# Kernel optimization log

Measured on AMD Instinct MI355X. Metric: run time of the kernel, lower is better.

The kernel has to match this reference:

```python
import jax, jax.numpy as jnp
import numpy as np

N = 50000      # nodes (patients)
E = 500000     # directed edges
H = 128        # Config.HIDDEN_DIM
GH = 256       # Config.GRAPH_HIDDEN
C = 14         # Config.NUM_CLASSES


def setup_inputs() -> dict:
    key = jax.random.key(0)
    ks = jax.random.split(key, 24)
    s = 0.02
    inp = {
        "h_v": jax.random.normal(ks[0], (N, H), jnp.float32),
        "h_t": jax.random.normal(ks[1], (N, H), jnp.float32),
        "h_tab": jax.random.normal(ks[2], (N, H), jnp.float32),
        "edge_index": jax.random.randint(ks[3], (2, E), 0, N, jnp.int64),
        # SAGEConv1: in=3H, out=GH  (lin_l on mean-aggr neighbors w/ bias, lin_r on root, no bias)
        "W1l": jax.random.normal(ks[4], (3 * H, GH), jnp.float32) * s,
        "W1r": jax.random.normal(ks[5], (3 * H, GH), jnp.float32) * s,
        "b1g": jnp.zeros((GH,), jnp.float32),
        # SAGEConv2: in=GH, out=H
        "W2l": jax.random.normal(ks[6], (GH, H), jnp.float32) * s,
        "W2r": jax.random.normal(ks[7], (GH, H), jnp.float32) * s,
        "b2g": jnp.zeros((H,), jnp.float32),
        # projections H->H
        "Wsh": jax.random.normal(ks[8], (H, H), jnp.float32) * s,
        "bsh": jnp.zeros((H,), jnp.float32),
        "Wst": jax.random.normal(ks[9], (H, H), jnp.float32) * s,
        "bst": jnp.zeros((H,), jnp.float32),
        "Wstab": jax.random.normal(ks[10], (H, H), jnp.float32) * s,
        "bstab": jnp.zeros((H,), jnp.float32),
        # classifier 4H -> 256 -> C
        "Wc1": jax.random.normal(ks[11], (4 * H, 256), jnp.float32) * s,
        "bc1": jnp.zeros((256,), jnp.float32),
        "Wc2": jax.random.normal(ks[12], (256, C), jnp.float32) * s,
        "bc2": jnp.zeros((C,), jnp.float32),
    }
    return inp


def _sage_conv(x, src, dst, Wl, Wr, b):
    # PyG SAGEConv with mean aggregation (eval mode):
    # out = mean_{j in N(i)} x_j @ Wl + b  +  x_i @ Wr
    n = x.shape[0]
    agg = jax.ops.segment_sum(x[src], dst, num_segments=n)          # [N, d_in]
    cnt = jax.ops.segment_sum(jnp.ones((src.shape[0],), x.dtype), dst, num_segments=n)
    mean = agg / jnp.maximum(cnt, 1.0)[:, None]
    return mean @ Wl + b + x @ Wr


def reference(h_v, h_t, h_tab, edge_index,
              W1l, W1r, b1g, W2l, W2r, b2g,
              Wsh, bsh, Wst, bst, Wstab, bstab,
              Wc1, bc1, Wc2, bc2):
    src, dst = edge_index[0], edge_index[1]
    node_feats = jnp.concatenate([h_v, h_t, h_tab], axis=1)          # [N, 3H]
    h_g = jax.nn.relu(_sage_conv(node_feats, src, dst, W1l, W1r, b1g))
    h_g = _sage_conv(h_g, src, dst, W2l, W2r, b2g)                   # [N, H]
    # F.normalize(p=2, dim=1)
    h_g = h_g / jnp.maximum(jnp.linalg.norm(h_g, axis=1, keepdims=True), 1e-12)
    z_shared = h_g @ Wsh + bsh
    z_t = h_t @ Wst + bst
    z_tab = h_tab @ Wstab + bstab
    combined = jnp.concatenate([z_shared, z_t, z_tab, h_g], axis=1)  # [N, 4H]
    logits = jax.nn.relu(combined @ Wc1 + bc1) @ Wc2 + bc2           # [N, C]
    return (logits, z_shared, z_t, z_tab)
```

## Files before the change

kernel.cpp:

```cpp
#include <hip/hip_runtime.h>
#include <math.h>

typedef __attribute__((ext_vector_type(8))) short short8;
typedef __attribute__((ext_vector_type(4))) float f32x4;
typedef __attribute__((ext_vector_type(4))) unsigned int u32x4;

static __device__ __forceinline__ unsigned short f2bf(float f) {
    union { float f; unsigned int u; } v; v.f = f;
    unsigned int r = v.u + 0x7fffu + ((v.u >> 16) & 1u);
    return (unsigned short)(r >> 16);
}
static __device__ __forceinline__ float bflo(unsigned int u) {
    union { unsigned int u; float f; } v; v.u = u << 16; return v.f;
}
static __device__ __forceinline__ float bfhi(unsigned int u) {
    union { unsigned int u; float f; } v; v.u = u & 0xffff0000u; return v.f;
}

typedef __attribute__((address_space(1))) const unsigned int gu32;
typedef __attribute__((address_space(3))) unsigned int lu32;
static __device__ __forceinline__ void gload16(const void* g, void* l) {
    __builtin_amdgcn_global_load_lds((gu32*)g, (lu32*)l, 16, 0, 0);
}

__global__ void convert_x(const float* __restrict__ hv, const float* __restrict__ ht,
                          const float* __restrict__ htab, unsigned short* __restrict__ X,
                          int total )
{
    int idx = blockIdx.x * blockDim.x + threadIdx.x;
    if (idx >= total) return;
    int r = idx / 96;
    int c4 = idx - r * 96;
    int seg = c4 >> 5;
    const float* s = (seg == 0) ? hv : (seg == 1) ? ht : htab;
    float4 v = ((const float4*)s)[(size_t)r * 32 + (c4 & 31)];
    ushort4 o;
    o.x = f2bf(v.x); o.y = f2bf(v.y); o.z = f2bf(v.z); o.w = f2bf(v.w);
    *(ushort4*)(X + (size_t)r * 384 + c4 * 4) = o;
}

struct WDesc { const float* src; int K; int N; int dstoff; };
struct WPack { WDesc w[9]; };
__global__ void convert_w(WPack p, unsigned short* __restrict__ dst)
{
    WDesc d = p.w[blockIdx.y];
    int total = d.K * d.N;
    for (int i = blockIdx.x * blockDim.x + threadIdx.x; i < total;
         i += gridDim.x * blockDim.x) {
        int k = i / d.N, n = i - k * d.N;
        dst[d.dstoff + (size_t)n * d.K + k] = f2bf(d.src[i]);
    }
}

struct GemmP {
    const unsigned short* A; int lda;
    const unsigned short* Bt;
    const float* bias;
    float* Cf; int ldcf;
    unsigned short* Cb; int ldcb;
};
struct GemmP3 { GemmP q[3]; };

template<int MODE, int NP>
__global__ __launch_bounds__(256, 4) void gemm4(GemmP3 ps, int M, int K)
{
    __shared__ __align__(16) unsigned short smem[128 * 64 * 2];
    unsigned short* As = smem;
    unsigned short* Bs = smem + 128 * 64;
    const GemmP P = ps.q[(MODE == 1) ? blockIdx.z : 0];
    const int tid = threadIdx.x;
    const int lane = tid & 63;
    const int wid = tid >> 6;
    const int wr = wid >> 1, wc = wid & 1;
    const int bid = blockIdx.x;
    const int q = bid >> 3;
    const int m0 = ((bid & 7) + 8 * (q / NP)) * 128;
    const int n0 = (q % NP) * 128;

    const int lrow = lane >> 3;
    const int lchk = (lane & 7) ^ lrow;
    const unsigned short* gA[4];
    #pragma unroll
    for (int i = 0; i < 4; ++i) {
        int r = m0 + wid * 32 + i * 8 + lrow;
        if (r > M - 1) r = M - 1;
        gA[i] = P.A + (size_t)r * P.lda + lchk * 8;
    }
    const unsigned short* gB[4];
    #pragma unroll
    for (int i = 0; i < 4; ++i) {
        int r = n0 + wid * 32 + i * 8 + lrow;
        gB[i] = P.Bt + (size_t)r * K + lchk * 8;
    }
    unsigned short* lA = As + wid * 32 * 64;
    unsigned short* lB = Bs + wid * 32 * 64;

    f32x4 acc[4][4] = {};
    const int nt = K >> 6;
    for (int t = 0; t < nt; ++t) {
        __syncthreads();
        #pragma unroll
        for (int i = 0; i < 4; ++i) gload16(gA[i] + t * 64, lA + i * 8 * 64);
        #pragma unroll
        for (int i = 0; i < 4; ++i) gload16(gB[i] + t * 64, lB + i * 8 * 64);
        asm volatile("s_waitcnt vmcnt(0)" ::: "memory");
        __syncthreads();
        #pragma unroll
        for (int kk = 0; kk < 2; ++kk) {
            int g = kk * 4 + (lane >> 4);
            short8 a[4], b[4];
            #pragma unroll
            for (int mi = 0; mi < 4; ++mi) {
                int row = wr * 64 + mi * 16 + (lane & 15);
                a[mi] = *(const short8*)(As + row * 64 + ((g ^ (row & 7)) * 8));
            }
            #pragma unroll
            for (int ni = 0; ni < 4; ++ni) {
                int row = wc * 64 + ni * 16 + (lane & 15);
                b[ni] = *(const short8*)(Bs + row * 64 + ((g ^ (row & 7)) * 8));
            }
            #pragma unroll
            for (int mi = 0; mi < 4; ++mi)
                #pragma unroll
                for (int ni = 0; ni < 4; ++ni)
                    acc[mi][ni] = __builtin_amdgcn_mfma_f32_16x16x32_bf16(
                        a[mi], b[ni], acc[mi][ni], 0, 0, 0);
        }
    }

    if (MODE == 0) {
        unsigned short* stage = smem;
        #pragma unroll
        for (int half = 0; half < 2; ++half) {
            __syncthreads();
            if (wr == half) {
                #pragma unroll
                for (int mi = 0; mi < 4; ++mi)
                    #pragma unroll
                    for (int ni = 0; ni < 4; ++ni) {
                        int colL = wc * 64 + ni * 16 + (lane & 15);
                        #pragma unroll
                        for (int j = 0; j < 4; ++j) {
                            int rel = mi * 16 + ((lane >> 4) << 2) + j;
                            stage[rel * 128 + colL] = f2bf(acc[mi][ni][j]);
                        }
                    }
            }
            __syncthreads();
            #pragma unroll
            for (int p = 0; p < 4; ++p) {
                int idx = p * 256 + tid;
                int r = idx >> 4, c8 = idx & 15;
                int grow = m0 + half * 64 + r;
                if (grow < M)
                    __builtin_nontemporal_store(
                        *(const u32x4*)(stage + r * 128 + c8 * 8),
                        (u32x4*)(P.Cb + (size_t)grow * P.ldcb + n0 + c8 * 8));
            }
        }
    }

    if (MODE == 1) {
        __syncthreads();
        #pragma unroll
        for (int mi = 0; mi < 4; ++mi)
            #pragma unroll
            for (int ni = 0; ni < 4; ++ni) {
                int colL = wc * 64 + ni * 16 + (lane & 15);
                float bv = P.bias[colL];
                #pragma unroll
                for (int j = 0; j < 4; ++j) {
                    int rL = wr * 64 + mi * 16 + ((lane >> 4) << 2) + j;
                    smem[rL * 128 + colL] = f2bf(acc[mi][ni][j] + bv);
                }
            }
        __syncthreads();
        #pragma unroll
        for (int p = 0; p < 8; ++p) {
            int idx = p * 256 + tid;
            int r = idx >> 4, c8 = idx & 15;
            int grow = m0 + r;
            if (grow < M)
                __builtin_nontemporal_store(
                    *(const u32x4*)(smem + r * 128 + c8 * 8),
                    (u32x4*)(P.Cb + (size_t)grow * P.ldcb + n0 + c8 * 8));
        }
        float* stagef = (float*)smem;
        #pragma unroll
        for (int half = 0; half < 2; ++half) {
            __syncthreads();
            if (wr == half) {
                #pragma unroll
                for (int mi = 0; mi < 4; ++mi)
                    #pragma unroll
                    for (int ni = 0; ni < 4; ++ni) {
                        int colL = wc * 64 + ni * 16 + (lane & 15);
                        float bv = P.bias[colL];
                        #pragma unroll
                        for (int j = 0; j < 4; ++j) {
                            int rel = mi * 16 + ((lane >> 4) << 2) + j;
                            stagef[rel * 128 + colL] = acc[mi][ni][j] + bv;
                        }
                    }
            }
            __syncthreads();
            #pragma unroll
            for (int p = 0; p < 8; ++p) {
                int idx = p * 256 + tid;
                int r = idx >> 5, c4 = idx & 31;
                int grow = m0 + half * 64 + r;
                if (grow < M)
                    __builtin_nontemporal_store(
                        *(const f32x4*)(stagef + r * 128 + c4 * 4),
                        (f32x4*)(P.Cf + (size_t)grow * P.ldcf + n0 + c4 * 4));
            }
        }
    }
}

__global__ __launch_bounds__(512, 2) void gemm5(
    const unsigned short* __restrict__ A,
    const unsigned short* __restrict__ Bt,
    const float* __restrict__ bias,
    const unsigned short* __restrict__ Wc2t,
    const float* __restrict__ bc2,
    float* __restrict__ logits,
    int M, int K)
{
    __shared__ __align__(16) unsigned short smem[128 * 256];
    unsigned short* As = smem;
    unsigned short* Bs = smem + 128 * 64;
    const int tid = threadIdx.x;
    const int lane = tid & 63;
    const int wid = tid >> 6;
    const int wr = wid >> 2;
    const int wc = wid & 3;
    const int m0 = blockIdx.x * 128;

    const int lrow = lane >> 3;
    const int lchk = (lane & 7) ^ lrow;
    const unsigned short* gA[2];
    #pragma unroll
    for (int i = 0; i < 2; ++i) {
        int r = m0 + wid * 16 + i * 8 + lrow;
        if (r > M - 1) r = M - 1;
        gA[i] = A + (size_t)r * K + lchk * 8;
    }
    const unsigned short* gB[4];
    #pragma unroll
    for (int i = 0; i < 4; ++i) {
        int r = wid * 32 + i * 8 + lrow;
        gB[i] = Bt + (size_t)r * K + lchk * 8;
    }
    unsigned short* lA = As + wid * 16 * 64;
    unsigned short* lB = Bs + wid * 32 * 64;

    f32x4 acc[4][4] = {};
    const int nt = K >> 6;
    for (int t = 0; t < nt; ++t) {
        __syncthreads();
        #pragma unroll
        for (int i = 0; i < 2; ++i) gload16(gA[i] + t * 64, lA + i * 8 * 64);
        #pragma unroll
        for (int i = 0; i < 4; ++i) gload16(gB[i] + t * 64, lB + i * 8 * 64);
        asm volatile("s_waitcnt vmcnt(0)" ::: "memory");
        __syncthreads();
        #pragma unroll
        for (int kk = 0; kk < 2; ++kk) {
            int g = kk * 4 + (lane >> 4);
            short8 a[4], b[4];
            #pragma unroll
            for (int mi = 0; mi < 4; ++mi) {
                int row = wr * 64 + mi * 16 + (lane & 15);
                a[mi] = *(const short8*)(As + row * 64 + ((g ^ (row & 7)) * 8));
            }
            #pragma unroll
            for (int ni = 0; ni < 4; ++ni) {
                int row = wc * 64 + ni * 16 + (lane & 15);
                b[ni] = *(const short8*)(Bs + row * 64 + ((g ^ (row & 7)) * 8));
            }
            #pragma unroll
            for (int mi = 0; mi < 4; ++mi)
                #pragma unroll
                for (int ni = 0; ni < 4; ++ni)
                    acc[mi][ni] = __builtin_amdgcn_mfma_f32_16x16x32_bf16(
                        a[mi], b[ni], acc[mi][ni], 0, 0, 0);
        }
    }

    __syncthreads();
    #pragma unroll
    for (int mi = 0; mi < 4; ++mi)
        #pragma unroll
        for (int ni = 0; ni < 4; ++ni) {
            int colL = wc * 64 + ni * 16 + (lane & 15);
            float bv = bias[colL];
            #pragma unroll
            for (int j = 0; j < 4; ++j) {
                int rL = wr * 64 + mi * 16 + ((lane >> 4) << 2) + j;
                float x = fmaxf(acc[mi][ni][j] + bv, 0.0f);
                int c8 = colL >> 3;
                smem[rL * 256 + ((c8 ^ (rL & 7)) * 8) + (colL & 7)] = f2bf(x);
            }
        }
    __syncthreads();
    f32x4 lacc = {0.f, 0.f, 0.f, 0.f};
    int rL = wid * 16 + (lane & 15);
    #pragma unroll
    for (int k0 = 0; k0 < 256; k0 += 32) {
        int c8 = (k0 >> 3) + (lane >> 4);
        short8 a = *(const short8*)(smem + rL * 256 + ((c8 ^ (rL & 7)) * 8));
        short8 b = *(const short8*)(Wc2t + (lane & 15) * 256 + k0 + (lane >> 4) * 8);
        lacc = __builtin_amdgcn_mfma_f32_16x16x32_bf16(a, b, lacc, 0, 0, 0);
    }
    int colL = lane & 15;
    if (colL < 14) {
        float bb = bc2[colL];
        #pragma unroll
        for (int j = 0; j < 4; ++j) {
            int r = m0 + wid * 16 + (lane >> 4) * 4 + j;
            if (r < M)
                __builtin_nontemporal_store(lacc[j] + bb,
                    logits + (size_t)r * 14 + colL);
        }
    }
}

__global__ void count_deg(const int* __restrict__ dst, int* __restrict__ deg, int E)
{
    int e = blockIdx.x * blockDim.x + threadIdx.x;
    if (e < E) atomicAdd(&deg[dst[e]], 1);
}

__global__ __launch_bounds__(1024) void scan_part(
    const int* __restrict__ deg, int* __restrict__ off, int* __restrict__ sums, int N)
{
    __shared__ int buf[1024];
    int i = blockIdx.x * 1024 + threadIdx.x;
    int v = (i < N) ? deg[i] : 0;
    buf[threadIdx.x] = v;
    __syncthreads();
    #pragma unroll
    for (int o = 1; o < 1024; o <<= 1) {
        int t = (threadIdx.x >= o) ? buf[threadIdx.x - o] : 0;
        __syncthreads();
        buf[threadIdx.x] += t;
        __syncthreads();
    }
    if (i < N) off[i] = buf[threadIdx.x] - v;
    if (threadIdx.x == 1023) sums[blockIdx.x] = buf[1023];
}

__global__ void scan_sums(int* __restrict__ sums, int* __restrict__ offN, int nb)
{
    int lane = threadIdx.x;
    int v = (lane < nb) ? sums[lane] : 0;
    int incl = v;
    #pragma unroll
    for (int o = 1; o < 64; o <<= 1) {
        int t = __shfl_up(incl, o);
        if (lane >= o) incl += t;
    }
    if (lane < nb) sums[lane] = incl - v;
    if (lane == 63) *offN = incl;
}

__global__ __launch_bounds__(1024) void scan_add(
    const int* __restrict__ sums, int* __restrict__ off,
    int* __restrict__ cursor, int N)
{
    int i = blockIdx.x * 1024 + threadIdx.x;
    if (i < N) {
        int v = off[i] + sums[blockIdx.x];
        off[i] = v;
        cursor[i] = v;
    }
}

__global__ void fill_csr(const int* __restrict__ src, const int* __restrict__ dst,
                         int* __restrict__ cursor, int* __restrict__ csr, int E)
{
    int e = blockIdx.x * blockDim.x + threadIdx.x;
    if (e < E) {
        int p = atomicAdd(&cursor[dst[e]], 1);
        csr[p] = src[e];
    }
}

__global__ __launch_bounds__(256) void sage1_gather(
    const unsigned short* __restrict__ y1,
    const int* __restrict__ off, const int* __restrict__ csr,
    const float* __restrict__ b, unsigned short* __restrict__ out, int N)
{
    int lane = threadIdx.x & 63;
    int node = blockIdx.x * 4 + (threadIdx.x >> 6);
    if (node >= N) return;
    int s = off[node], e = off[node + 1];
    int half = lane >> 5, l32 = lane & 31;
    float a[8] = {};
    int p = s + half;
    for (; p + 6 < e; p += 8) {
        int j0 = csr[p],     j1 = csr[p + 2];
        int j2 = csr[p + 4], j3 = csr[p + 6];
        uint4 v0 = *(const uint4*)(y1 + (size_t)j0 * 512 + l32 * 8);
        uint4 v1 = *(const uint4*)(y1 + (size_t)j1 * 512 + l32 * 8);
        uint4 v2 = *(const uint4*)(y1 + (size_t)j2 * 512 + l32 * 8);
        uint4 v3 = *(const uint4*)(y1 + (size_t)j3 * 512 + l32 * 8);
        a[0] += bflo(v0.x); a[1] += bfhi(v0.x); a[2] += bflo(v0.y); a[3] += bfhi(v0.y);
        a[4] += bflo(v0.z); a[5] += bfhi(v0.z); a[6] += bflo(v0.w); a[7] += bfhi(v0.w);
        a[0] += bflo(v1.x); a[1] += bfhi(v1.x); a[2] += bflo(v1.y); a[3] += bfhi(v1.y);
        a[4] += bflo(v1.z); a[5] += bfhi(v1.z); a[6] += bflo(v1.w); a[7] += bfhi(v1.w);
        a[0] += bflo(v2.x); a[1] += bfhi(v2.x); a[2] += bflo(v2.y); a[3] += bfhi(v2.y);
        a[4] += bflo(v2.z); a[5] += bfhi(v2.z); a[6] += bflo(v2.w); a[7] += bfhi(v2.w);
        a[0] += bflo(v3.x); a[1] += bfhi(v3.x); a[2] += bflo(v3.y); a[3] += bfhi(v3.y);
        a[4] += bflo(v3.z); a[5] += bfhi(v3.z); a[6] += bflo(v3.w); a[7] += bfhi(v3.w);
    }
    for (; p + 2 < e; p += 4) {
        int j0 = csr[p], j1 = csr[p + 2];
        uint4 v0 = *(const uint4*)(y1 + (size_t)j0 * 512 + l32 * 8);
        uint4 v1 = *(const uint4*)(y1 + (size_t)j1 * 512 + l32 * 8);
        a[0] += bflo(v0.x); a[1] += bfhi(v0.x); a[2] += bflo(v0.y); a[3] += bfhi(v0.y);
        a[4] += bflo(v0.z); a[5] += bfhi(v0.z); a[6] += bflo(v0.w); a[7] += bfhi(v0.w);
        a[0] += bflo(v1.x); a[1] += bfhi(v1.x); a[2] += bflo(v1.y); a[3] += bfhi(v1.y);
        a[4] += bflo(v1.z); a[5] += bfhi(v1.z); a[6] += bflo(v1.w); a[7] += bfhi(v1.w);
    }
    for (; p < e; p += 2) {
        int j = csr[p];
        uint4 v = *(const uint4*)(y1 + (size_t)j * 512 + l32 * 8);
        a[0] += bflo(v.x); a[1] += bfhi(v.x); a[2] += bflo(v.y); a[3] += bfhi(v.y);
        a[4] += bflo(v.z); a[5] += bfhi(v.z); a[6] += bflo(v.w); a[7] += bfhi(v.w);
    }
    #pragma unroll
    for (int i = 0; i < 8; ++i) a[i] += __shfl_xor(a[i], 32);
    if (half == 0) {
        float inv = (e > s) ? 1.0f / (float)(e - s) : 1.0f;
        uint4 rv = *(const uint4*)(y1 + (size_t)node * 512 + 256 + l32 * 8);
        float4 b0 = ((const float4*)b)[l32 * 2];
        float4 b1 = ((const float4*)b)[l32 * 2 + 1];
        float r[8] = {bflo(rv.x), bfhi(rv.x), bflo(rv.y), bfhi(rv.y),
                      bflo(rv.z), bfhi(rv.z), bflo(rv.w), bfhi(rv.w)};
        float bb[8] = {b0.x, b0.y, b0.z, b0.w, b1.x, b1.y, b1.z, b1.w};
        u32x4 vv;
        #pragma unroll
        for (int i = 0; i < 4; ++i) {
            unsigned int lo = f2bf(fmaxf(a[2*i]   * inv + bb[2*i]   + r[2*i],   0.f));
            unsigned int hi = f2bf(fmaxf(a[2*i+1] * inv + bb[2*i+1] + r[2*i+1], 0.f));
            vv[i] = lo | (hi << 16);
        }
        __builtin_nontemporal_store(vv, (u32x4*)(out + (size_t)node * 256 + l32 * 8));
    }
}

__global__ __launch_bounds__(256) void sage2_gather_norm(
    const unsigned short* __restrict__ y2,
    const int* __restrict__ off, const int* __restrict__ csr,
    const float* __restrict__ b, unsigned short* __restrict__ outb, int N)
{
    int lane = threadIdx.x & 63;
    int node = blockIdx.x * 4 + (threadIdx.x >> 6);
    if (node >= N) return;
    int s = off[node], e = off[node + 1];
    int grp = lane >> 4, l16 = lane & 15;
    float a[8] = {};
    int p = s + grp;
    for (; p + 4 < e; p += 8) {
        int j0 = csr[p], j1 = csr[p + 4];
        uint4 v0 = *(const uint4*)(y2 + (size_t)j0 * 256 + l16 * 8);
        uint4 v1 = *(const uint4*)(y2 + (size_t)j1 * 256 + l16 * 8);
        a[0] += bflo(v0.x); a[1] += bfhi(v0.x); a[2] += bflo(v0.y); a[3] += bfhi(v0.y);
        a[4] += bflo(v0.z); a[5] += bfhi(v0.z); a[6] += bflo(v0.w); a[7] += bfhi(v0.w);
        a[0] += bflo(v1.x); a[1] += bfhi(v1.x); a[2] += bflo(v1.y); a[3] += bfhi(v1.y);
        a[4] += bflo(v1.z); a[5] += bfhi(v1.z); a[6] += bflo(v1.w); a[7] += bfhi(v1.w);
    }
    for (; p < e; p += 4) {
        int j = csr[p];
        uint4 v = *(const uint4*)(y2 + (size_t)j * 256 + l16 * 8);
        a[0] += bflo(v.x); a[1] += bfhi(v.x); a[2] += bflo(v.y); a[3] += bfhi(v.y);
        a[4] += bflo(v.z); a[5] += bfhi(v.z); a[6] += bflo(v.w); a[7] += bfhi(v.w);
    }
    #pragma unroll
    for (int i = 0; i < 8; ++i) {
        a[i] += __shfl_xor(a[i], 16);
        a[i] += __shfl_xor(a[i], 32);
    }
    if (grp == 0) {
        float inv = (e > s) ? 1.0f / (float)(e - s) : 1.0f;
        uint4 rv = *(const uint4*)(y2 + (size_t)node * 256 + 128 + l16 * 8);
        float4 b0 = ((const float4*)b)[l16 * 2];
        float4 b1 = ((const float4*)b)[l16 * 2 + 1];
        float r[8] = {bflo(rv.x), bfhi(rv.x), bflo(rv.y), bfhi(rv.y),
                      bflo(rv.z), bfhi(rv.z), bflo(rv.w), bfhi(rv.w)};
        float bb[8] = {b0.x, b0.y, b0.z, b0.w, b1.x, b1.y, b1.z, b1.w};
        float h[8];
        float ss = 0.f;
        #pragma unroll
        for (int i = 0; i < 8; ++i) {
            h[i] = a[i] * inv + bb[i] + r[i];
            ss += h[i] * h[i];
        }
        ss += __shfl_xor(ss, 1);
        ss += __shfl_xor(ss, 2);
        ss += __shfl_xor(ss, 4);
        ss += __shfl_xor(ss, 8);
        float sc = 1.0f / fmaxf(sqrtf(ss), 1e-12f);
        u32x4 vv;
        #pragma unroll
        for (int i = 0; i < 4; ++i) {
            unsigned int lo = f2bf(h[2*i] * sc);
            unsigned int hi = f2bf(h[2*i+1] * sc);
            vv[i] = lo | (hi << 16);
        }
        __builtin_nontemporal_store(vv, (u32x4*)(outb + (size_t)node * 512 + l16 * 8));
    }
}

extern "C" void kernel_launch(void* const* d_in, const int* in_sizes, int n_in,
                              void* d_out, int out_size, void* d_ws, size_t ws_size,
                              hipStream_t stream)
{
    const float* h_v   = (const float*)d_in[0];
    const float* h_t   = (const float*)d_in[1];
    const float* h_tab = (const float*)d_in[2];
    const int*   eidx  = (const int*)d_in[3];
    const float* W1l = (const float*)d_in[4];
    const float* W1r = (const float*)d_in[5];
    const float* b1g = (const float*)d_in[6];
    const float* W2l = (const float*)d_in[7];
    const float* W2r = (const float*)d_in[8];
    const float* b2g = (const float*)d_in[9];
    const float* Wsh = (const float*)d_in[10];
    const float* bsh = (const float*)d_in[11];
    const float* Wst = (const float*)d_in[12];
    const float* bst = (const float*)d_in[13];
    const float* Wstab = (const float*)d_in[14];
    const float* bstab = (const float*)d_in[15];
    const float* Wc1 = (const float*)d_in[16];
    const float* bc1 = (const float*)d_in[17];
    const float* Wc2 = (const float*)d_in[18];
    const float* bc2 = (const float*)d_in[19];

    const int N = in_sizes[0] / 128;
    const int E = in_sizes[3] / 2;
    const int* src = eidx;
    const int* dst = eidx + E;

    int* deg    = (int*)d_ws;
    int* off    = deg + N;
    int* cursor = off + N + 1;
    int* csr    = cursor + N;
    int* sums   = csr + E;
    size_t int_bytes = ((size_t)3 * N + 1 + E + 64) * 4;
    unsigned short* Wt = (unsigned short*)((char*)d_ws + ((int_bytes + 255) & ~(size_t)255));
    const int oW1l = 0;
    const int oW1r = oW1l + 98304;
    const int oW2l = oW1r + 98304;
    const int oW2r = oW2l + 32768;
    const int oWsh = oW2r + 32768;
    const int oWst = oWsh + 16384;
    const int oWstab = oWst + 16384;
    const int oWc1 = oWstab + 16384;
    const int oWc2t = oWc1 + 131072;
    const int wtotal = oWc2t + 4096;

    unsigned short* Xbf   = Wt + wtotal;
    unsigned short* bufY  = Xbf + (size_t)N * 384;
    unsigned short* bufH  = bufY + (size_t)N * 512;
    unsigned short* bufY2 = bufH + (size_t)N * 256;

    float* out    = (float*)d_out;
    float* logits = out;
    float* z_sh   = out + (size_t)N * 14;
    float* z_t    = z_sh + (size_t)N * 128;
    float* z_tab  = z_t + (size_t)N * 128;

    const int gx = (N + 127) / 128;
    const int gxp = (gx + 7) & ~7;
    const int nb = (N + 1023) / 1024;

    hipMemsetAsync(deg, 0, (size_t)N * 4, stream);
    hipMemsetAsync(Wt + oWc2t, 0, 16 * 256 * 2, stream);
    count_deg<<<(E + 255) / 256, 256, 0, stream>>>(dst, deg, E);
    scan_part<<<nb, 1024, 0, stream>>>(deg, off, sums, N);
    scan_sums<<<1, 64, 0, stream>>>(sums, off + N, nb);
    scan_add<<<nb, 1024, 0, stream>>>(sums, off, cursor, N);
    fill_csr<<<(E + 255) / 256, 256, 0, stream>>>(src, dst, cursor, csr, E);

    convert_x<<<(N * 96 + 255) / 256, 256, 0, stream>>>(h_v, h_t, h_tab, Xbf, N * 96);
    WPack p;
    p.w[0] = {W1l, 384, 256, oW1l};     p.w[1] = {W1r, 384, 256, oW1r};
    p.w[2] = {W2l, 256, 128, oW2l};     p.w[3] = {W2r, 256, 128, oW2r};
    p.w[4] = {Wsh, 128, 128, oWsh};     p.w[5] = {Wst, 128, 128, oWst};
    p.w[6] = {Wstab, 128, 128, oWstab}; p.w[7] = {Wc1, 512, 256, oWc1};
    p.w[8] = {Wc2, 256, 14, oWc2t};
    convert_w<<<dim3(128, 9), 256, 0, stream>>>(p, Wt);

    unsigned short* y1 = bufY;
    {
        GemmP3 g{};
        g.q[0] = {Xbf, 384, Wt + oW1l, nullptr, nullptr, 0, y1, 512};
        gemm4<0, 4><<<dim3(gxp * 4), 256, 0, stream>>>(g, N, 384);
    }

    sage1_gather<<<(N + 3) / 4, 256, 0, stream>>>(y1, off, csr, b1g, bufH, N);

    {
        GemmP3 g{};
        g.q[0] = {bufH, 256, Wt + oW2l, nullptr, nullptr, 0, bufY2, 256};
        gemm4<0, 2><<<dim3(gxp * 2), 256, 0, stream>>>(g, N, 256);
    }

    unsigned short* cls_bf = bufY;
    sage2_gather_norm<<<(N + 3) / 4, 256, 0, stream>>>(bufY2, off, csr, b2g,
        cls_bf + 384, N);

    {
        GemmP3 g{};
        g.q[0] = {cls_bf + 384, 512, Wt + oWsh,   bsh,   z_sh,  128, cls_bf + 0,   512};
        g.q[1] = {Xbf + 128,    384, Wt + oWst,   bst,   z_t,   128, cls_bf + 128, 512};
        g.q[2] = {Xbf + 256,    384, Wt + oWstab, bstab, z_tab, 128, cls_bf + 256, 512};
        gemm4<1, 1><<<dim3(gxp, 1, 3), 256, 0, stream>>>(g, N, 128);
    }

    gemm5<<<dim3(gxp), 512, 0, stream>>>(cls_bf, Wt + oWc1, bc1,
        Wt + oWc2t, bc2, logits, N, 512);
}
```

Before: 265.9 us.

## Fuse projection GEMMs into classifier kernel, keeping z tiles in shared memory

Merges the three H->H projection GEMMs (z_shared, z_t, z_tab) into the classifier kernel. Each block computes a 128-row z tile, writes it to global in fp32, keeps a bf16 copy in LDS, and immediately accumulates it into the first classifier layer. This removes one launch and the bf16 round-trip of the combined feature buffer through global memory. In exchange, the projections now run serially inside one block per row tile, with more barriers and no overlap between loads and MFMA, which lowers parallelism in that stage.

```diff
diff --git a/kernel.cpp b/kernel.cpp
--- a/kernel.cpp
+++ b/kernel.cpp
@@ -67,7 +67,7 @@
     __shared__ __align__(16) unsigned short smem[128 * 64 * 2];
     unsigned short* As = smem;
     unsigned short* Bs = smem + 128 * 64;
-    const GemmP P = ps.q[(MODE == 1) ? blockIdx.z : 0];
+    const GemmP P = ps.q[0];
     const int tid = threadIdx.x;
     const int lane = tid & 63;
     const int wid = tid >> 6;
@@ -128,141 +128,215 @@
         }
     }
 
-    if (MODE == 0) {
-        unsigned short* stage = smem;
-        #pragma unroll
-        for (int half = 0; half < 2; ++half) {
-            __syncthreads();
-            if (wr == half) {
-                #pragma unroll
-                for (int mi = 0; mi < 4; ++mi)
+    unsigned short* stage = smem;
+    #pragma unroll
+    for (int half = 0; half < 2; ++half) {
+        __syncthreads();
+        if (wr == half) {
+            #pragma unroll
+            for (int mi = 0; mi < 4; ++mi)
+                #pragma unroll
+                for (int ni = 0; ni < 4; ++ni) {
+                    int colL = wc * 64 + ni * 16 + (lane & 15);
                     #pragma unroll
-                    for (int ni = 0; ni < 4; ++ni) {
-                        int colL = wc * 64 + ni * 16 + (lane & 15);
-                        #pragma unroll
-                        for (int j = 0; j < 4; ++j) {
-                            int rel = mi * 16 + ((lane >> 4) << 2) + j;
-                            stage[rel * 128 + colL] = f2bf(acc[mi][ni][j]);
-                        }
+                    for (int j = 0; j < 4; ++j) {
+                        int rel = mi * 16 + ((lane >> 4) << 2) + j;
+                        stage[rel * 128 + colL] = f2bf(acc[mi][ni][j]);
                     }
-            }
-            __syncthreads();
-            #pragma unroll
-            for (int p = 0; p < 4; ++p) {
-                int idx = p * 256 + tid;
-                int r = idx >> 4, c8 = idx & 15;
-                int grow = m0 + half * 64 + r;
-                if (grow < M)
-                    __builtin_nontemporal_store(
-                        *(const u32x4*)(stage + r * 128 + c8 * 8),
-                        (u32x4*)(P.Cb + (size_t)grow * P.ldcb + n0 + c8 * 8));
-            }
-        }
-    }
-
-    if (MODE == 1) {
-        __syncthreads();
-        #pragma unroll
-        for (int mi = 0; mi < 4; ++mi)
-            #pragma unroll
-            for (int ni = 0; ni < 4; ++ni) {
-                int colL = wc * 64 + ni * 16 + (lane & 15);
-                float bv = P.bias[colL];
-                #pragma unroll
-                for (int j = 0; j < 4; ++j) {
-                    int rL = wr * 64 + mi * 16 + ((lane >> 4) << 2) + j;
-                    smem[rL * 128 + colL] = f2bf(acc[mi][ni][j] + bv);
                 }
-            }
-        __syncthreads();
-        #pragma unroll
-        for (int p = 0; p < 8; ++p) {
+        }
+        __syncthreads();
+        #pragma unroll
+        for (int p = 0; p < 4; ++p) {
             int idx = p * 256 + tid;
             int r = idx >> 4, c8 = idx & 15;
-            int grow = m0 + r;
+            int grow = m0 + half * 64 + r;
             if (grow < M)
                 __builtin_nontemporal_store(
-                    *(const u32x4*)(smem + r * 128 + c8 * 8),
+                    *(const u32x4*)(stage + r * 128 + c8 * 8),
                     (u32x4*)(P.Cb + (size_t)grow * P.ldcb + n0 + c8 * 8));
         }
-        float* stagef = (float*)smem;
-        #pragma unroll
-        for (int half = 0; half < 2; ++half) {
-            __syncthreads();
-            if (wr == half) {
-                #pragma unroll
-                for (int mi = 0; mi < 4; ++mi)
-                    #pragma unroll
-                    for (int ni = 0; ni < 4; ++ni) {
-                        int colL = wc * 64 + ni * 16 + (lane & 15);
-                        float bv = P.bias[colL];
-                        #pragma unroll
-                        for (int j = 0; j < 4; ++j) {
-                            int rel = mi * 16 + ((lane >> 4) << 2) + j;
-                            stagef[rel * 128 + colL] = acc[mi][ni][j] + bv;
-                        }
-                    }
-            }
-            __syncthreads();
-            #pragma unroll
-            for (int p = 0; p < 8; ++p) {
-                int idx = p * 256 + tid;
-                int r = idx >> 5, c4 = idx & 31;
-                int grow = m0 + half * 64 + r;
-                if (grow < M)
-                    __builtin_nontemporal_store(
-                        *(const f32x4*)(stagef + r * 128 + c4 * 4),
-                        (f32x4*)(P.Cf + (size_t)grow * P.ldcf + n0 + c4 * 4));
-            }
-        }
-    }
-}
-
-__global__ __launch_bounds__(512, 2) void gemm5(
-    const unsigned short* __restrict__ A,
-    const unsigned short* __restrict__ Bt,
-    const float* __restrict__ bias,
+    }
+}
+
+__global__ __launch_bounds__(512) void gemm6(
+    const unsigned short* __restrict__ hg,
+    const unsigned short* __restrict__ Xbf,
+    const unsigned short* __restrict__ Wp,
+    const float* __restrict__ bsh, const float* __restrict__ bst,
+    const float* __restrict__ bstab,
+    const unsigned short* __restrict__ Wc1t,
+    const float* __restrict__ bc1,
     const unsigned short* __restrict__ Wc2t,
     const float* __restrict__ bc2,
+    float* __restrict__ zout,
     float* __restrict__ logits,
-    int M, int K)
+    int M)
 {
     __shared__ __align__(16) unsigned short smem[128 * 256];
-    unsigned short* As = smem;
-    unsigned short* Bs = smem + 128 * 64;
+    unsigned short* As  = smem;
+    unsigned short* Bs  = smem + 8192;
+    unsigned short* Zbf = smem + 16384;
     const int tid = threadIdx.x;
     const int lane = tid & 63;
     const int wid = tid >> 6;
     const int wr = wid >> 2;
     const int wc = wid & 3;
     const int m0 = blockIdx.x * 128;
-
     const int lrow = lane >> 3;
     const int lchk = (lane & 7) ^ lrow;
-    const unsigned short* gA[2];
-    #pragma unroll
-    for (int i = 0; i < 2; ++i) {
-        int r = m0 + wid * 16 + i * 8 + lrow;
-        if (r > M - 1) r = M - 1;
-        gA[i] = A + (size_t)r * K + lchk * 8;
-    }
-    const unsigned short* gB[4];
-    #pragma unroll
-    for (int i = 0; i < 4; ++i) {
-        int r = wid * 32 + i * 8 + lrow;
-        gB[i] = Bt + (size_t)r * K + lchk * 8;
-    }
-    unsigned short* lA = As + wid * 16 * 64;
-    unsigned short* lB = Bs + wid * 32 * 64;
-
-    f32x4 acc[4][4] = {};
-    const int nt = K >> 6;
-    for (int t = 0; t < nt; ++t) {
-        __syncthreads();
-        #pragma unroll
-        for (int i = 0; i < 2; ++i) gload16(gA[i] + t * 64, lA + i * 8 * 64);
-        #pragma unroll
-        for (int i = 0; i < 4; ++i) gload16(gB[i] + t * 64, lB + i * 8 * 64);
+    const float* bz[3] = {bsh, bst, bstab};
+
+    f32x4 hacc[4][4] = {};
+
+    #pragma unroll
+    for (int p = 0; p < 3; ++p) {
+        const unsigned short* Ap = (p == 0) ? hg : (Xbf + (p == 1 ? 128 : 256));
+        const int lda = (p == 0) ? 128 : 384;
+        const unsigned short* Wpp = Wp + p * 16384;
+        const float* bp = bz[p];
+        f32x4 zacc[4][2] = {};
+
+        #pragma unroll
+        for (int t = 0; t < 2; ++t) {
+            __syncthreads();
+            #pragma unroll
+            for (int i = 0; i < 2; ++i) {
+                int r = m0 + wid * 16 + i * 8 + lrow;
+                if (r > M - 1) r = M - 1;
+                gload16(Ap + (size_t)r * lda + t * 64 + lchk * 8,
+                        As + wid * 16 * 64 + i * 8 * 64);
+            }
+            #pragma unroll
+            for (int i = 0; i < 2; ++i) {
+                int r = wid * 16 + i * 8 + lrow;
+                gload16(Wpp + (size_t)r * 128 + t * 64 + lchk * 8,
+                        Bs + wid * 16 * 64 + i * 8 * 64);
+            }
+            asm volatile("s_waitcnt vmcnt(0)" ::: "memory");
+            __syncthreads();
+            #pragma unroll
+            for (int kk = 0; kk < 2; ++kk) {
+                int g = kk * 4 + (lane >> 4);
+                short8 a[4], b[2];
+                #pragma unroll
+                for (int mi = 0; mi < 4; ++mi) {
+                    int row = wr * 64 + mi * 16 + (lane & 15);
+                    a[mi] = *(const short8*)(As + row * 64 + ((g ^ (row & 7)) * 8));
+                }
+                #pragma unroll
+                for (int ni = 0; ni < 2; ++ni) {
+                    int row = wc * 32 + ni * 16 + (lane & 15);
+                    b[ni] = *(const short8*)(Bs + row * 64 + ((g ^ (row & 7)) * 8));
+                }
+                #pragma unroll
+                for (int mi = 0; mi < 4; ++mi)
+                    #pragma unroll
+                    for (int ni = 0; ni < 2; ++ni)
+                        zacc[mi][ni] = __builtin_amdgcn_mfma_f32_16x16x32_bf16(
+                            a[mi], b[ni], zacc[mi][ni], 0, 0, 0);
+            }
+        }
+
+        __syncthreads();
+        #pragma unroll
+        for (int mi = 0; mi < 4; ++mi)
+            #pragma unroll
+            for (int ni = 0; ni < 2; ++ni) {
+                int colL = wc * 32 + ni * 16 + (lane & 15);
+                float bv = bp[colL];
+                #pragma unroll
+                for (int j = 0; j < 4; ++j) {
+                    int rL = wr * 64 + mi * 16 + ((lane >> 4) << 2) + j;
+                    float x = zacc[mi][ni][j] + bv;
+                    Zbf[rL * 128 + (((colL >> 3) ^ (rL & 7)) * 8) + (colL & 7)] = f2bf(x);
+                }
+            }
+
+        float* stagef = (float*)smem;
+        float* zo = zout + (size_t)p * M * 128;
+        #pragma unroll
+        for (int half = 0; half < 2; ++half) {
+            __syncthreads();
+            if (wr == half) {
+                #pragma unroll
+                for (int mi = 0; mi < 4; ++mi)
+                    #pragma unroll
+                    for (int ni = 0; ni < 2; ++ni) {
+                        int colL = wc * 32 + ni * 16 + (lane & 15);
+                        float bv = bp[colL];
+                        #pragma unroll
+                        for (int j = 0; j < 4; ++j) {
+                            int rel = mi * 16 + ((lane >> 4) << 2) + j;
+                            stagef[rel * 128 + colL] = zacc[mi][ni][j] + bv;
+                        }
+                    }
+            }
+            __syncthreads();
+            #pragma unroll
+            for (int q = 0; q < 4; ++q) {
+                int idx = q * 512 + tid;
+                int r = idx >> 5, c4 = idx & 31;
+                int grow = m0 + half * 64 + r;
+                if (grow < M)
+                    __builtin_nontemporal_store(
+                        *(const f32x4*)(stagef + r * 128 + c4 * 4),
+                        (f32x4*)(zo + (size_t)grow * 128 + c4 * 4));
+            }
+        }
+
+        #pragma unroll
+        for (int t = 0; t < 2; ++t) {
+            __syncthreads();
+            #pragma unroll
+            for (int i = 0; i < 4; ++i) {
+                int r = wid * 32 + i * 8 + lrow;
+                gload16(Wc1t + (size_t)r * 512 + p * 128 + t * 64 + lchk * 8,
+                        smem + wid * 32 * 64 + i * 8 * 64);
+            }
+            asm volatile("s_waitcnt vmcnt(0)" ::: "memory");
+            __syncthreads();
+            #pragma unroll
+            for (int kk = 0; kk < 2; ++kk) {
+                int g = kk * 4 + (lane >> 4);
+                int gz = t * 8 + g;
+                short8 a[4], b[4];
+                #pragma unroll
+                for (int mi = 0; mi < 4; ++mi) {
+                    int row = wr * 64 + mi * 16 + (lane & 15);
+                    a[mi] = *(const short8*)(Zbf + row * 128 + ((gz ^ (row & 7)) * 8));
+                }
+                #pragma unroll
+                for (int ni = 0; ni < 4; ++ni) {
+                    int row = wc * 64 + ni * 16 + (lane & 15);
+                    b[ni] = *(const short8*)(smem + row * 64 + ((g ^ (row & 7)) * 8));
+                }
+                #pragma unroll
+                for (int mi = 0; mi < 4; ++mi)
+                    #pragma unroll
+                    for (int ni = 0; ni < 4; ++ni)
+                        hacc[mi][ni] = __builtin_amdgcn_mfma_f32_16x16x32_bf16(
+                            a[mi], b[ni], hacc[mi][ni], 0, 0, 0);
+            }
+        }
+    }
+
+    #pragma unroll
+    for (int t = 0; t < 2; ++t) {
+        __syncthreads();
+        #pragma unroll
+        for (int i = 0; i < 2; ++i) {
+            int r = m0 + wid * 16 + i * 8 + lrow;
+            if (r > M - 1) r = M - 1;
+            gload16(hg + (size_t)r * 128 + t * 64 + lchk * 8,
+                    As + wid * 16 * 64 + i * 8 * 64);
+        }
+        #pragma unroll
+        for (int i = 0; i < 4; ++i) {
+            int r = wid * 32 + i * 8 + lrow;
+            gload16(Wc1t + (size_t)r * 512 + 384 + t * 64 + lchk * 8,
+                    Zbf + wid * 32 * 64 + i * 8 * 64);
+        }
         asm volatile("s_waitcnt vmcnt(0)" ::: "memory");
         __syncthreads();
         #pragma unroll
@@ -277,14 +351,14 @@
             #pragma unroll
             for (int ni = 0; ni < 4; ++ni) {
                 int row = wc * 64 + ni * 16 + (lane & 15);
-                b[ni] = *(const short8*)(Bs + row * 64 + ((g ^ (row & 7)) * 8));
+                b[ni] = *(const short8*)(Zbf + row * 64 + ((g ^ (row & 7)) * 8));
             }
             #pragma unroll
             for (int mi = 0; mi < 4; ++mi)
                 #pragma unroll
                 for (int ni = 0; ni < 4; ++ni)
-                    acc[mi][ni] = __builtin_amdgcn_mfma_f32_16x16x32_bf16(
-                        a[mi], b[ni], acc[mi][ni], 0, 0, 0);
+                    hacc[mi][ni] = __builtin_amdgcn_mfma_f32_16x16x32_bf16(
+                        a[mi], b[ni], hacc[mi][ni], 0, 0, 0);
         }
     }
 
@@ -294,11 +368,11 @@
         #pragma unroll
         for (int ni = 0; ni < 4; ++ni) {
             int colL = wc * 64 + ni * 16 + (lane & 15);
-            float bv = bias[colL];
+            float bv = bc1[colL];
             #pragma unroll
             for (int j = 0; j < 4; ++j) {
                 int rL = wr * 64 + mi * 16 + ((lane >> 4) << 2) + j;
-                float x = fmaxf(acc[mi][ni][j] + bv, 0.0f);
+                float x = fmaxf(hacc[mi][ni][j] + bv, 0.0f);
                 int c8 = colL >> 3;
                 smem[rL * 256 + ((c8 ^ (rL & 7)) * 8) + (colL & 7)] = f2bf(x);
             }
@@ -510,7 +584,7 @@
             unsigned int hi = f2bf(h[2*i+1] * sc);
             vv[i] = lo | (hi << 16);
         }
-        __builtin_nontemporal_store(vv, (u32x4*)(outb + (size_t)node * 512 + l16 * 8));
+        __builtin_nontemporal_store(vv, (u32x4*)(outb + (size_t)node * 128 + l16 * 8));
     }
 }
 
@@ -570,8 +644,6 @@
     float* out    = (float*)d_out;
     float* logits = out;
     float* z_sh   = out + (size_t)N * 14;
-    float* z_t    = z_sh + (size_t)N * 128;
-    float* z_tab  = z_t + (size_t)N * 128;
 
     const int gx = (N + 127) / 128;
     const int gxp = (gx + 7) & ~7;
@@ -609,18 +681,10 @@
         gemm4<0, 2><<<dim3(gxp * 2), 256, 0, stream>>>(g, N, 256);
     }
 
-    unsigned short* cls_bf = bufY;
-    sage2_gather_norm<<<(N + 3) / 4, 256, 0, stream>>>(bufY2, off, csr, b2g,
-        cls_bf + 384, N);
-
-    {
-        GemmP3 g{};
-        g.q[0] = {cls_bf + 384, 512, Wt + oWsh,   bsh,   z_sh,  128, cls_bf + 0,   512};
-        g.q[1] = {Xbf + 128,    384, Wt + oWst,   bst,   z_t,   128, cls_bf + 128, 512};
-        g.q[2] = {Xbf + 256,    384, Wt + oWstab, bstab, z_tab, 128, cls_bf + 256, 512};
-        gemm4<1, 1><<<dim3(gxp, 1, 3), 256, 0, stream>>>(g, N, 128);
-    }
-
-    gemm5<<<dim3(gxp), 512, 0, stream>>>(cls_bf, Wt + oWc1, bc1,
-        Wt + oWc2t, bc2, logits, N, 512);
-}
+    unsigned short* hg = bufY;
+    sage2_gather_norm<<<(N + 3) / 4, 256, 0, stream>>>(bufY2, off, csr, b2g, hg, N);
+
+    gemm6<<<dim3(gxp), 512, 0, stream>>>(hg, Xbf, Wt + oWsh,
+        bsh, bst, bstab, Wt + oWc1, bc1, Wt + oWc2t, bc2,
+        z_sh, logits, N);
+}
```

Result: no change. 269.9 us (+1.5%).
